# Performance work log

Measured on AMD Instinct MI355X. Metric: run time of the kernel, lower is better.

Reference implementation:

```python
import jax, jax.numpy as jnp
import numpy as np

DIM = 2048
N_HEADS = 32
N_KV_HEADS = 8
HEAD_DIM = DIM // N_HEADS
ROPE_BASE = 10000.0
BATCH = 2
SEQ = 2048


def _rope_cos_sin(seq_len, dtype=jnp.float32):
    inv_freq = 1.0 / (ROPE_BASE ** (jnp.arange(0, HEAD_DIM, 2, dtype=jnp.float32) / HEAD_DIM))
    pos = jnp.arange(seq_len, dtype=jnp.float32)
    freqs = pos[:, None] * inv_freq[None, :]  # (seq, head_dim/2)
    return jnp.cos(freqs).astype(dtype), jnp.sin(freqs).astype(dtype)


def _apply_rope(x, cos, sin):
    # x: (b, h, s, d); cos/sin: (s, d/2). Interleaved (even/odd) RoPE.
    cos = cos[None, None, :, :]
    sin = sin[None, None, :, :]
    x_even = x[..., ::2]
    x_odd = x[..., 1::2]
    rot_even = x_even * cos - x_odd * sin
    rot_odd = x_even * sin + x_odd * cos
    out = jnp.stack((rot_even, rot_odd), axis=-1)
    return out.reshape(x.shape)


def setup_inputs() -> dict:
    key = jax.random.key(0)
    ks = jax.random.split(key, 5)
    s = 0.02
    return {
        "x": jax.random.normal(ks[0], (BATCH, SEQ, DIM), dtype=jnp.float32),
        "wq": jax.random.normal(ks[1], (DIM, N_HEADS * HEAD_DIM), dtype=jnp.float32) * s,
        "wk": jax.random.normal(ks[2], (DIM, N_KV_HEADS * HEAD_DIM), dtype=jnp.float32) * s,
        "wv": jax.random.normal(ks[3], (DIM, N_KV_HEADS * HEAD_DIM), dtype=jnp.float32) * s,
        "wo": jax.random.normal(ks[4], (DIM, DIM), dtype=jnp.float32) * s,
    }


def reference(x, wq, wk, wv, wo):
    b, s, _ = x.shape
    q = (x @ wq).reshape(b, s, N_HEADS, HEAD_DIM).transpose(0, 2, 1, 3)
    k = (x @ wk).reshape(b, s, N_KV_HEADS, HEAD_DIM).transpose(0, 2, 1, 3)
    v = (x @ wv).reshape(b, s, N_KV_HEADS, HEAD_DIM).transpose(0, 2, 1, 3)
    cos, sin = _rope_cos_sin(s, x.dtype)
    q = _apply_rope(q, cos, sin)
    k = _apply_rope(k, cos, sin)
    rep = N_HEADS // N_KV_HEADS
    if rep > 1:
        k = jnp.repeat(k, rep, axis=1)
        v = jnp.repeat(v, rep, axis=1)
    scores = jnp.einsum("bhqd,bhkd->bhqk", q, k) / (HEAD_DIM ** 0.5)
    causal = jnp.tril(jnp.ones((s, s), dtype=bool))
    scores = jnp.where(causal[None, None], scores, -jnp.inf)
    probs = jax.nn.softmax(scores, axis=-1)
    out = jnp.einsum("bhqk,bhkd->bhqd", probs, v)
    out = out.transpose(0, 2, 1, 3).reshape(b, s, DIM)
    return out @ wo
```

## Files before the change

kernel.cpp:

```cpp
#include <hip/hip_runtime.h>
#include <stdint.h>

#define DIM   2048
#define NH    32
#define NKV   8
#define HD    64
#define BATCH 2
#define SEQ   2048

typedef __attribute__((ext_vector_type(8))) short  short8;
typedef __attribute__((ext_vector_type(4))) short  short4v;
typedef __attribute__((ext_vector_type(4))) float  f32x4;

#if __has_builtin(__builtin_amdgcn_exp2f)
#define EXP2(x) __builtin_amdgcn_exp2f(x)
#else
#define EXP2(x) exp2f(x)
#endif

static __device__ __forceinline__ short f2bf(float f) {
  union { float f; uint32_t u; } v; v.f = f;
  uint32_t r = v.u + 0x7FFFu + ((v.u >> 16) & 1u);
  return (short)(r >> 16);
}

static __device__ __forceinline__ uint32_t cvtpk_bf16(float lo, float hi) {
  uint32_t r;
  asm("v_cvt_pk_bf16_f32 %0, %1, %2" : "=v"(r) : "v"(lo), "v"(hi));
  return r;
}

#define GLD16(gp, lp) __builtin_amdgcn_global_load_lds(                      \
    (__attribute__((address_space(1))) void*)(void*)(gp),                    \
    (__attribute__((address_space(3))) void*)(lp), 16, 0, 0)

#define QSCALE 0.1803368801111244f


__global__ void cvt_x_kernel(const float* __restrict__ in, short* __restrict__ out, int n4) {
  int i = blockIdx.x * blockDim.x + threadIdx.x;
  if (i < n4) {
    f32x4 v = *reinterpret_cast<const f32x4*>(in + (size_t)i * 4);
    short4v o;
    o.x = f2bf(v.x); o.y = f2bf(v.y); o.z = f2bf(v.z); o.w = f2bf(v.w);
    *reinterpret_cast<short4v*>(out + (size_t)i * 4) = o;
  }
}

__global__ void transpose_bf_kernel(const float* __restrict__ in, short* __restrict__ out,
                                    int R, int C) {
  __shared__ float t[32][33];
  int c0 = blockIdx.x * 32, r0 = blockIdx.y * 32;
  int tx = threadIdx.x, ty = threadIdx.y;
#pragma unroll
  for (int j = 0; j < 32; j += 8)
    t[ty + j][tx] = in[(size_t)(r0 + ty + j) * C + c0 + tx];
  __syncthreads();
#pragma unroll
  for (int j = 0; j < 32; j += 8)
    out[(size_t)(c0 + ty + j) * R + r0 + tx] = f2bf(t[tx][ty + j]);
}

__global__ void rope_tab_kernel(float* __restrict__ ct, float* __restrict__ st) {
  int i = blockIdx.x * blockDim.x + threadIdx.x;
  if (i < SEQ * 32) {
    int pos = i >> 5, f = i & 31;
    float inv = powf(10000.0f, -(float)f / 32.0f);
    float th = (float)pos * inv;
    ct[i] = cosf(th);
    st[i] = sinf(th);
  }
}


__device__ __forceinline__ void mfma_tile(const short* __restrict__ as_,
                                          const short* __restrict__ bs_,
                                          int wr, int wc, int lg, int lr,
                                          f32x4 (&acc)[4][4]) {
  short8 af[4], bq[4];
#pragma unroll
  for (int mt = 0; mt < 4; ++mt) {
    int row = wr * 64 + mt * 16 + lr;
    af[mt] = *(const short8*)&as_[row * 32 + ((lg ^ ((row >> 1) & 3)) << 3)];
  }
#pragma unroll
  for (int nt = 0; nt < 4; ++nt) {
    int row = wc * 64 + nt * 16 + lr;
    bq[nt] = *(const short8*)&bs_[row * 32 + ((lg ^ ((row >> 1) & 3)) << 3)];
  }
  __builtin_amdgcn_s_setprio(1);
#pragma unroll
  for (int mt = 0; mt < 4; ++mt)
#pragma unroll
    for (int nt = 0; nt < 4; ++nt)
      acc[mt][nt] = __builtin_amdgcn_mfma_f32_16x16x32_bf16(af[mt], bq[nt], acc[mt][nt], 0, 0, 0);
  __builtin_amdgcn_s_setprio(0);
}

#define STAGE4(SA, SB) do {                                                  \
    GLD16(pA0, (SA) + w * 512);  GLD16(pA1, (SA) + 2048 + w * 512);          \
    GLD16(pB0, (SB) + w * 512);  GLD16(pB1, (SB) + 2048 + w * 512);          \
    pA0 += 32; pA1 += 32; pB0 += 32; pB1 += 32; } while (0)

#define TILE(CA, CB, SA, SB, DOSTAGE, VM) do {                               \
    asm volatile("s_waitcnt vmcnt(" VM ")" ::: "memory");                    \
    __builtin_amdgcn_s_barrier();                                            \
    __builtin_amdgcn_sched_barrier(0);                                       \
    if (DOSTAGE) { STAGE4(SA, SB); }                                         \
    mfma_tile(CA, CB, wr, wc, lg, lr, acc);                                  \
  } while (0)

__device__ __forceinline__ void gemm_mainloop(const short* __restrict__ A,
                                              const short* __restrict__ Bt,
                                              int m0, int n0,
                                              short* As, short* Bs,
                                              f32x4 (&acc)[4][4]) {
  const int tid = threadIdx.x;
  const int w = tid >> 6, l = tid & 63;
  const int lg = l >> 4, lr = l & 15;
  const int wr = w >> 1, wc = w & 1;
  const int c1 = tid + 256;
  const int r0 = tid >> 2, k0 = ((tid & 3) ^ ((r0 >> 1) & 3)) << 3;
  const int r1 = c1 >> 2,  k1 = ((c1 & 3) ^ ((r1 >> 1) & 3)) << 3;
  const short* pA0 = A + (size_t)(m0 + r0) * DIM + k0;
  const short* pA1 = A + (size_t)(m0 + r1) * DIM + k1;
  const short* pB0 = Bt + (size_t)(n0 + r0) * DIM + k0;
  const short* pB1 = Bt + (size_t)(n0 + r1) * DIM + k1;
  short* A0 = As;            short* B0 = Bs;
  short* A1 = As + 4096;     short* B1 = Bs + 4096;
  short* A2 = As + 8192;     short* B2 = Bs + 8192;

  STAGE4(A0, B0);
  STAGE4(A1, B1);

  for (int it = 0; it < 20; ++it) {
    TILE(A0, B0, A2, B2, true, "4");
    TILE(A1, B1, A0, B0, true, "4");
    TILE(A2, B2, A1, B1, true, "4");
  }
  TILE(A0, B0, A2, B2, true,  "4");
  TILE(A1, B1, A0, B0, true,  "4");
  TILE(A2, B2, A0, B0, false, "4");
  TILE(A0, B0, A1, B1, false, "0");
}

__device__ __forceinline__ int2 xcd_swizzle(int nwg) {
  int id = blockIdx.y * gridDim.x + blockIdx.x;
  int swz = (id & 7) * (nwg >> 3) + (id >> 3);
  return make_int2(swz % gridDim.x, swz / gridDim.x);
}

__global__ void __launch_bounds__(256, 3)
gemm_qkv_kernel(const short* __restrict__ A,
                const short* __restrict__ wqt, const short* __restrict__ wkt,
                const short* __restrict__ wvt,
                short* __restrict__ q_ws, short* __restrict__ k_ws, short* __restrict__ v_ws,
                const float* __restrict__ ct, const float* __restrict__ st) {
  __shared__ __align__(16) short As[12288];
  __shared__ __align__(16) short Bs[12288];
  int2 bxy = xcd_swizzle(24 * 32);
  const int n0g = bxy.x * 128;
  const int m0 = bxy.y * 128;
  int mode, n0;
  const short* Bt;
  short* outp;
  if (n0g < 2048)      { mode = 1; Bt = wqt; n0 = n0g;        outp = q_ws; }
  else if (n0g < 2560) { mode = 2; Bt = wkt; n0 = n0g - 2048; outp = k_ws; }
  else                 { mode = 3; Bt = wvt; n0 = n0g - 2560; outp = v_ws; }

  f32x4 acc[4][4] = {};
  gemm_mainloop(A, Bt, m0, n0, As, Bs, acc);

  const int tid = threadIdx.x;
  const int w = tid >> 6, l = tid & 63;
  const int lg = l >> 4, lr = l & 15;
  const int wr = w >> 1, wc = w & 1;
  const int mrow0 = m0 + wr * 64;
  const int ncol0 = n0 + wc * 64;
#pragma unroll
  for (int mt = 0; mt < 4; ++mt)
#pragma unroll
    for (int nt = 0; nt < 4; ++nt)
#pragma unroll
      for (int i = 0; i < 4; ++i) {
        int m = mrow0 + mt * 16 + lg * 4 + i;
        int n = ncol0 + nt * 16 + lr;
        float v = acc[mt][nt][i];
        int b = m >> 11, s = m & (SEQ - 1);
        int h = n >> 6, d = n & 63;
        if (mode == 3) {
          outp[((size_t)(b * NKV + h) * HD + d) * SEQ + s] = f2bf(v);
        } else {
          float p = __shfl_xor(v, 1);
          float cs = ct[(s << 5) + (d >> 1)];
          float sn = st[(s << 5) + (d >> 1)];
          float r = ((d & 1) == 0) ? (v * cs - p * sn) : (p * sn + v * cs);
          if (mode == 1) {
            r *= QSCALE;
            outp[((size_t)(b * NH + h) * SEQ + s) * HD + d] = f2bf(r);
          } else {
            outp[((size_t)(b * NKV + h) * SEQ + s) * HD + d] = f2bf(r);
          }
        }
      }
}

__global__ void __launch_bounds__(256, 3)
gemm_o_kernel(const short* __restrict__ A, const short* __restrict__ Bt,
              float* __restrict__ out) {
  __shared__ __align__(16) short As[12288];
  __shared__ __align__(16) short Bs[12288];
  int2 bxy = xcd_swizzle(16 * 32);
  const int m0 = bxy.y * 128, n0 = bxy.x * 128;
  f32x4 acc[4][4] = {};
  gemm_mainloop(A, Bt, m0, n0, As, Bs, acc);
  const int tid = threadIdx.x;
  const int w = tid >> 6, l = tid & 63;
  const int lg = l >> 4, lr = l & 15;
  const int wr = w >> 1, wc = w & 1;
#pragma unroll
  for (int mt = 0; mt < 4; ++mt)
#pragma unroll
    for (int nt = 0; nt < 4; ++nt)
#pragma unroll
      for (int i = 0; i < 4; ++i) {
        int m = m0 + wr * 64 + mt * 16 + lg * 4 + i;
        int n = n0 + wc * 64 + nt * 16 + lr;
        out[(size_t)m * DIM + n] = acc[mt][nt][i];
      }
}

__global__ void __launch_bounds__(256, 3)
attn_fwd_kernel(const short* __restrict__ Q, const short* __restrict__ K,
                const short* __restrict__ V, short* __restrict__ O) {
  __shared__ __align__(16) short Ks[3][4096];
  __shared__ __align__(16) short Vs[3][4096];
  const int tid = threadIdx.x;
  const int w = tid >> 6, l = tid & 63;
  const int lg = l >> 4, lr = l & 15;
  const int h = blockIdx.y;
  const int b = blockIdx.z;
  const int kvh = h >> 2;
  const int lh = lg >> 1, sub = (lg & 1) << 2;

  const short* kbase = K + (size_t)(b * NKV + kvh) * SEQ * HD;
  const short* vbase = V + (size_t)(b * NKV + kvh) * HD * SEQ;

  const int c1 = tid + 256;
  const int r0 = tid >> 3, e0 = ((tid & 7) ^ (r0 & 7)) << 3;
  const int r1 = c1 >> 3, e1 = ((c1 & 7) ^ (r1 & 7)) << 3;

  short8 ones;
#pragma unroll
  for (int i = 0; i < 8; ++i) ones[i] = (short)0x3F80;

#define ASTAGE(kvt, KB, VB) do { const int kv_ = (kvt) * 64;                  \
    GLD16(kbase + (size_t)(kv_ + r0) * HD + e0, (KB) + w * 512);              \
    GLD16(kbase + (size_t)(kv_ + r1) * HD + e1, (KB) + 2048 + w * 512);       \
    GLD16(vbase + (size_t)r0 * SEQ + kv_ + e0, (VB) + w * 512);               \
    GLD16(vbase + (size_t)r1 * SEQ + kv_ + e1, (VB) + 2048 + w * 512); } while (0)

  for (int qi = 0; qi < 2; ++qi) {
    const int qblk = (qi == 0) ? (int)blockIdx.x : (31 - (int)blockIdx.x);
    const int q0 = qblk * 64;
    const int qrow = q0 + w * 16 + lr;

    const short* qptr = Q + ((size_t)(b * NH + h) * SEQ + qrow) * HD;
    short8 qf0 = *(const short8*)(qptr + (lg << 3));
    short8 qf1 = *(const short8*)(qptr + 32 + (lg << 3));

    float m_run = 0.f;
    f32x4 oacc[4] = {};
    f32x4 lacc = {};

    short* kb0 = Ks[0]; short* kb1 = Ks[1]; short* kb2 = Ks[2];
    short* vb0 = Vs[0]; short* vb1 = Vs[1]; short* vb2 = Vs[2];

    ASTAGE(0, kb0, vb0);
    if (qblk >= 1) ASTAGE(1, kb1, vb1);

    for (int t = 0; t <= qblk; ++t) {
      if (t < qblk) asm volatile("s_waitcnt vmcnt(4)" ::: "memory");
      else          asm volatile("s_waitcnt vmcnt(0)" ::: "memory");
      __builtin_amdgcn_s_barrier();
      __builtin_amdgcn_sched_barrier(0);
      if (t + 2 <= qblk) ASTAGE(t + 2, kb2, vb2);

      const short* ks = kb0;
      const short* vs = vb0;
      const int kv0 = t * 64;

      short8 ka[4][2];
#pragma unroll
      for (int t4 = 0; t4 < 4; ++t4) {
        int row = t4 * 16 + lr, rx = row & 7;
        ka[t4][0] = *(const short8*)&ks[row * 64 + ((lg ^ rx) << 3)];
        ka[t4][1] = *(const short8*)&ks[row * 64 + (((4 + lg) ^ rx) << 3)];
      }
      short8 vbf[4][2];
#pragma unroll
      for (int nt = 0; nt < 4; ++nt) {
        int row = nt * 16 + lr, rx = row & 7;
#pragma unroll
        for (int ks_ = 0; ks_ < 2; ++ks_) {
          union { short8 s8; short4v hh[2]; } u;
          u.hh[0] = *(const short4v*)&vs[row * 64 + (((4 * ks_ + lh) ^ rx) << 3) + sub];
          u.hh[1] = *(const short4v*)&vs[row * 64 + (((4 * ks_ + 2 + lh) ^ rx) << 3) + sub];
          vbf[nt][ks_] = u.s8;
        }
      }

      f32x4 sacc[4];
      {
        f32x4 seed;
        seed[0] = -m_run; seed[1] = -m_run; seed[2] = -m_run; seed[3] = -m_run;
        __builtin_amdgcn_s_setprio(1);
#pragma unroll
        for (int t4 = 0; t4 < 4; ++t4) {
          f32x4 z = __builtin_amdgcn_mfma_f32_16x16x32_bf16(ka[t4][0], qf0, seed, 0, 0, 0);
          sacc[t4] = __builtin_amdgcn_mfma_f32_16x16x32_bf16(ka[t4][1], qf1, z, 0, 0, 0);
        }
        __builtin_amdgcn_s_setprio(0);
      }

      if (t == qblk) {
#pragma unroll
        for (int t4 = 0; t4 < 4; ++t4)
#pragma unroll
          for (int i = 0; i < 4; ++i)
            if (kv0 + t4 * 16 + lg * 4 + i > qrow) sacc[t4][i] = -__builtin_inff();
      }

      float a0 = fmaxf(fmaxf(sacc[0][0], sacc[0][1]), sacc[0][2]);
      float a1 = fmaxf(fmaxf(sacc[0][3], sacc[1][0]), sacc[1][1]);
      float a2 = fmaxf(fmaxf(sacc[1][2], sacc[1][3]), sacc[2][0]);
      float a3 = fmaxf(fmaxf(sacc[2][1], sacc[2][2]), sacc[2][3]);
      float a4 = fmaxf(fmaxf(sacc[3][0], sacc[3][1]), sacc[3][2]);
      float tm = fmaxf(fmaxf(fmaxf(a0, a1), a2), fmaxf(fmaxf(a3, a4), sacc[3][3]));
      tm = fmaxf(tm, __shfl_xor(tm, 16));
      tm = fmaxf(tm, __shfl_xor(tm, 32));

      if (!__all(tm <= 12.0f)) {
        float d = fmaxf(tm, 0.f);
        float alpha = EXP2(-d);
        float av0 = __shfl(alpha, (lg << 2));
        float av1 = __shfl(alpha, (lg << 2) | 1);
        float av2 = __shfl(alpha, (lg << 2) | 2);
        float av3 = __shfl(alpha, (lg << 2) | 3);
#pragma unroll
        for (int nt = 0; nt < 4; ++nt) {
          oacc[nt][0] *= av0; oacc[nt][1] *= av1;
          oacc[nt][2] *= av2; oacc[nt][3] *= av3;
        }
        lacc[0] *= av0; lacc[1] *= av1; lacc[2] *= av2; lacc[3] *= av3;
        m_run += d;
#pragma unroll
        for (int t4 = 0; t4 < 4; ++t4)
#pragma unroll
          for (int i = 0; i < 4; ++i) sacc[t4][i] -= d;
      }

      union { short8 s8; uint32_t u[4]; } pa0, pa1;
      pa0.u[0] = cvtpk_bf16(EXP2(sacc[0][0]), EXP2(sacc[0][1]));
      pa0.u[1] = cvtpk_bf16(EXP2(sacc[0][2]), EXP2(sacc[0][3]));
      pa0.u[2] = cvtpk_bf16(EXP2(sacc[1][0]), EXP2(sacc[1][1]));
      pa0.u[3] = cvtpk_bf16(EXP2(sacc[1][2]), EXP2(sacc[1][3]));
      pa1.u[0] = cvtpk_bf16(EXP2(sacc[2][0]), EXP2(sacc[2][1]));
      pa1.u[1] = cvtpk_bf16(EXP2(sacc[2][2]), EXP2(sacc[2][3]));
      pa1.u[2] = cvtpk_bf16(EXP2(sacc[3][0]), EXP2(sacc[3][1]));
      pa1.u[3] = cvtpk_bf16(EXP2(sacc[3][2]), EXP2(sacc[3][3]));

      __builtin_amdgcn_s_setprio(1);
#pragma unroll
      for (int nt = 0; nt < 4; ++nt) {
        oacc[nt] = __builtin_amdgcn_mfma_f32_16x16x32_bf16(pa0.s8, vbf[nt][0], oacc[nt], 0, 0, 0);
        oacc[nt] = __builtin_amdgcn_mfma_f32_16x16x32_bf16(pa1.s8, vbf[nt][1], oacc[nt], 0, 0, 0);
      }
      lacc = __builtin_amdgcn_mfma_f32_16x16x32_bf16(pa0.s8, ones, lacc, 0, 0, 0);
      lacc = __builtin_amdgcn_mfma_f32_16x16x32_bf16(pa1.s8, ones, lacc, 0, 0, 0);
      __builtin_amdgcn_s_setprio(0);

      short* tk = kb0; kb0 = kb1; kb1 = kb2; kb2 = tk;
      short* tv = vb0; vb0 = vb1; vb1 = vb2; vb2 = tv;
    }

    float linv0 = 1.f / lacc[0], linv1 = 1.f / lacc[1];
    float linv2 = 1.f / lacc[2], linv3 = 1.f / lacc[3];
#pragma unroll
    for (int nt = 0; nt < 4; ++nt) {
      int d = nt * 16 + lr;
      int qb = q0 + w * 16 + lg * 4;
      O[(size_t)(b * SEQ + qb + 0) * DIM + h * HD + d] = f2bf(oacc[nt][0] * linv0);
      O[(size_t)(b * SEQ + qb + 1) * DIM + h * HD + d] = f2bf(oacc[nt][1] * linv1);
      O[(size_t)(b * SEQ + qb + 2) * DIM + h * HD + d] = f2bf(oacc[nt][2] * linv2);
      O[(size_t)(b * SEQ + qb + 3) * DIM + h * HD + d] = f2bf(oacc[nt][3] * linv3);
    }
    __syncthreads();
  }
#undef ASTAGE
}


extern "C" void kernel_launch(void* const* d_in, const int* in_sizes, int n_in,
                              void* d_out, int out_size, void* d_ws, size_t ws_size,
                              hipStream_t stream) {
  const float* x  = (const float*)d_in[0];
  const float* wq = (const float*)d_in[1];
  const float* wk = (const float*)d_in[2];
  const float* wv = (const float*)d_in[3];
  const float* wo = (const float*)d_in[4];
  float* out = (float*)d_out;
  char* ws = (char*)d_ws;

  short* x_bf  = (short*)(ws + 0);
  short* attn  = (short*)(ws + 0);
  short* q_ws  = (short*)(ws + 16777216);
  short* k_ws  = (short*)(ws + 33554432);
  short* v_ws  = (short*)(ws + 37748736);
  short* wq_t  = (short*)(ws + 41943040);
  short* wo_t  = (short*)(ws + 41943040);
  short* wk_t  = (short*)(ws + 50331648);
  short* wv_t  = (short*)(ws + 52428800);
  float* ct    = (float*)(ws + 54525952);
  float* st    = (float*)(ws + 54788096);
  (void)ws_size; (void)in_sizes; (void)n_in; (void)out_size;

  dim3 tb(32, 8);
  cvt_x_kernel<<<8192, 256, 0, stream>>>(x, x_bf, 2097152);
  transpose_bf_kernel<<<dim3(64, 64), tb, 0, stream>>>(wq, wq_t, DIM, 2048);
  transpose_bf_kernel<<<dim3(16, 64), tb, 0, stream>>>(wk, wk_t, DIM, 512);
  transpose_bf_kernel<<<dim3(16, 64), tb, 0, stream>>>(wv, wv_t, DIM, 512);
  rope_tab_kernel<<<256, 256, 0, stream>>>(ct, st);

  gemm_qkv_kernel<<<dim3(24, 32), 256, 0, stream>>>(x_bf, wq_t, wk_t, wv_t,
                                                    q_ws, k_ws, v_ws, ct, st);

  attn_fwd_kernel<<<dim3(16, 32, 2), 256, 0, stream>>>(q_ws, k_ws, v_ws, attn);

  transpose_bf_kernel<<<dim3(64, 64), tb, 0, stream>>>(wo, wo_t, DIM, 2048);
  gemm_o_kernel<<<dim3(16, 32), 256, 0, stream>>>(attn, wo_t, out);
}
```

Before: 221.6 us.

## Replace GEMM mainloop with 8-wave 256-wide tiles and 4-phase double-buffered schedule

Both projection GEMMs switch from 128x128 tiles with 4 waves and a triple-buffered K=32 pipeline to larger tiles (256x256 for QKV, 128x256 for O) with 8 waves and K=64 double buffering. Each K step is split into four phases that interleave LDS fragment reads, global prefetch and MFMA quadrants under barriers. The larger tiles give more operand reuse per LDS load and fewer global reads. In exchange, LDS use and register pressure per block rise and the grids get smaller (192 and 256 blocks), which may underfill the 256 CUs and lower occupancy.

```diff
diff --git a/kernel.cpp b/kernel.cpp
--- a/kernel.cpp
+++ b/kernel.cpp
@@ -73,75 +73,109 @@
 }
 
 
-__device__ __forceinline__ void mfma_tile(const short* __restrict__ as_,
-                                          const short* __restrict__ bs_,
-                                          int wr, int wc, int lg, int lr,
-                                          f32x4 (&acc)[4][4]) {
-  short8 af[4], bq[4];
-#pragma unroll
-  for (int mt = 0; mt < 4; ++mt) {
-    int row = wr * 64 + mt * 16 + lr;
-    af[mt] = *(const short8*)&as_[row * 32 + ((lg ^ ((row >> 1) & 3)) << 3)];
-  }
-#pragma unroll
-  for (int nt = 0; nt < 4; ++nt) {
-    int row = wc * 64 + nt * 16 + lr;
-    bq[nt] = *(const short8*)&bs_[row * 32 + ((lg ^ ((row >> 1) & 3)) << 3)];
-  }
-  __builtin_amdgcn_s_setprio(1);
-#pragma unroll
-  for (int mt = 0; mt < 4; ++mt)
-#pragma unroll
-    for (int nt = 0; nt < 4; ++nt)
-      acc[mt][nt] = __builtin_amdgcn_mfma_f32_16x16x32_bf16(af[mt], bq[nt], acc[mt][nt], 0, 0, 0);
-  __builtin_amdgcn_s_setprio(0);
-}
-
-#define STAGE4(SA, SB) do {                                                  \
-    GLD16(pA0, (SA) + w * 512);  GLD16(pA1, (SA) + 2048 + w * 512);          \
-    GLD16(pB0, (SB) + w * 512);  GLD16(pB1, (SB) + 2048 + w * 512);          \
-    pA0 += 32; pA1 += 32; pB0 += 32; pB1 += 32; } while (0)
-
-#define TILE(CA, CB, SA, SB, DOSTAGE, VM) do {                               \
-    asm volatile("s_waitcnt vmcnt(" VM ")" ::: "memory");                    \
-    __builtin_amdgcn_s_barrier();                                            \
-    __builtin_amdgcn_sched_barrier(0);                                       \
-    if (DOSTAGE) { STAGE4(SA, SB); }                                         \
-    mfma_tile(CA, CB, wr, wc, lg, lr, acc);                                  \
-  } while (0)
-
-__device__ __forceinline__ void gemm_mainloop(const short* __restrict__ A,
-                                              const short* __restrict__ Bt,
-                                              int m0, int n0,
-                                              short* As, short* Bs,
-                                              f32x4 (&acc)[4][4]) {
+template <int BM, int BN, int WN>
+__device__ __forceinline__ void gemm_8ph(const short* __restrict__ A,
+                                         const short* __restrict__ Bt,
+                                         int m0, int n0,
+                                         short* __restrict__ As,
+                                         short* __restrict__ Bs,
+                                         f32x4 (&acc)[BM / ((8 / WN) * 16)][BN / (WN * 16)]) {
+  constexpr int WM = 8 / WN;
+  constexpr int MREP = BM / (WM * 16);
+  constexpr int NREP = BN / (WN * 16);
+  constexpr int MR2 = MREP / 2, NR2 = NREP / 2;
+  constexpr int APASS = BM / 64, BPASS = BN / 64;
+  constexpr int ABUF = BM * 64, BBUF = BN * 64;
+  constexpr int NT = DIM / 64;
+
   const int tid = threadIdx.x;
   const int w = tid >> 6, l = tid & 63;
   const int lg = l >> 4, lr = l & 15;
-  const int wr = w >> 1, wc = w & 1;
-  const int c1 = tid + 256;
-  const int r0 = tid >> 2, k0 = ((tid & 3) ^ ((r0 >> 1) & 3)) << 3;
-  const int r1 = c1 >> 2,  k1 = ((c1 & 3) ^ ((r1 >> 1) & 3)) << 3;
-  const short* pA0 = A + (size_t)(m0 + r0) * DIM + k0;
-  const short* pA1 = A + (size_t)(m0 + r1) * DIM + k1;
-  const short* pB0 = Bt + (size_t)(n0 + r0) * DIM + k0;
-  const short* pB1 = Bt + (size_t)(n0 + r1) * DIM + k1;
-  short* A0 = As;            short* B0 = Bs;
-  short* A1 = As + 4096;     short* B1 = Bs + 4096;
-  short* A2 = As + 8192;     short* B2 = Bs + 8192;
-
-  STAGE4(A0, B0);
-  STAGE4(A1, B1);
-
-  for (int it = 0; it < 20; ++it) {
-    TILE(A0, B0, A2, B2, true, "4");
-    TILE(A1, B1, A0, B0, true, "4");
-    TILE(A2, B2, A1, B1, true, "4");
+  const int wr = w / WN, wc = w % WN;
+  const int srow = tid >> 3;
+  const int su2 = (tid & 7) ^ (srow & 7);
+  const short* pA0 = A + (size_t)(m0 + srow) * DIM + su2 * 8;
+  const short* pB0 = Bt + (size_t)(n0 + srow) * DIM + su2 * 8;
+
+  auto stageA = [&](int t, int buf) {
+#pragma unroll
+    for (int p = 0; p < APASS; ++p)
+      GLD16(pA0 + (size_t)p * 64 * DIM + t * 64, As + buf * ABUF + p * 4096 + w * 512);
+  };
+  auto stageB = [&](int t, int buf) {
+#pragma unroll
+    for (int p = 0; p < BPASS; ++p)
+      GLD16(pB0 + (size_t)p * 64 * DIM + t * 64, Bs + buf * BBUF + p * 4096 + w * 512);
+  };
+
+  short8 af[MR2][2], bf0[NR2][2], bf1[NR2][2];
+
+  auto readA = [&](int mh, const short* base) {
+#pragma unroll
+    for (int i = 0; i < MR2; ++i) {
+      const int row = wr * (MREP * 16) + (mh * MR2 + i) * 16 + lr;
+#pragma unroll
+      for (int kk = 0; kk < 2; ++kk)
+        af[i][kk] = *(const short8*)&base[row * 64 + (((kk * 4 + lg) ^ (row & 7)) << 3)];
+    }
+  };
+  auto readB = [&](short8 (&bf)[NR2][2], int nh, const short* base) {
+#pragma unroll
+    for (int j = 0; j < NR2; ++j) {
+      const int row = wc * (NREP * 16) + (nh * NR2 + j) * 16 + lr;
+#pragma unroll
+      for (int kk = 0; kk < 2; ++kk)
+        bf[j][kk] = *(const short8*)&base[row * 64 + (((kk * 4 + lg) ^ (row & 7)) << 3)];
+    }
+  };
+  auto mmaQ = [&](short8 (&bf)[NR2][2], int mh, int nh) {
+    __builtin_amdgcn_s_setprio(1);
+#pragma unroll
+    for (int i = 0; i < MR2; ++i)
+#pragma unroll
+      for (int j = 0; j < NR2; ++j)
+#pragma unroll
+        for (int kk = 0; kk < 2; ++kk)
+          acc[mh * MR2 + i][nh * NR2 + j] = __builtin_amdgcn_mfma_f32_16x16x32_bf16(
+              af[i][kk], bf[j][kk], acc[mh * MR2 + i][nh * NR2 + j], 0, 0, 0);
+    __builtin_amdgcn_s_setprio(0);
+  };
+
+#define PH_SYNC do { __builtin_amdgcn_s_barrier();                           \
+    asm volatile("s_waitcnt lgkmcnt(0)" ::: "memory");                       \
+    __builtin_amdgcn_sched_barrier(0); } while (0)
+
+  stageA(0, 0);
+  stageB(0, 0);
+  asm volatile("s_waitcnt vmcnt(0)" ::: "memory");
+  __builtin_amdgcn_s_barrier();
+
+  for (int t = 0; t < NT; ++t) {
+    const int cur = t & 1;
+    const short* ab = As + cur * ABUF;
+    const short* bb = Bs + cur * BBUF;
+    const bool more = (t + 1 < NT);
+    readA(0, ab);
+    readB(bf0, 0, bb);
+    if (more) stageA(t + 1, cur ^ 1);
+    PH_SYNC;
+    mmaQ(bf0, 0, 0);
+    __builtin_amdgcn_s_barrier();
+    readB(bf1, 1, bb);
+    if (more) stageB(t + 1, cur ^ 1);
+    PH_SYNC;
+    mmaQ(bf1, 0, 1);
+    __builtin_amdgcn_s_barrier();
+    readA(1, ab);
+    PH_SYNC;
+    mmaQ(bf0, 1, 0);
+    __builtin_amdgcn_s_barrier();
+    PH_SYNC;
+    mmaQ(bf1, 1, 1);
+    asm volatile("s_waitcnt vmcnt(0)" ::: "memory");
+    __builtin_amdgcn_s_barrier();
   }
-  TILE(A0, B0, A2, B2, true,  "4");
-  TILE(A1, B1, A0, B0, true,  "4");
-  TILE(A2, B2, A0, B0, false, "4");
-  TILE(A0, B0, A1, B1, false, "0");
+#undef PH_SYNC
 }
 
 __device__ __forceinline__ int2 xcd_swizzle(int nwg) {
@@ -150,17 +184,17 @@
   return make_int2(swz % gridDim.x, swz / gridDim.x);
 }
 
-__global__ void __launch_bounds__(256, 3)
+__global__ void __launch_bounds__(512, 2)
 gemm_qkv_kernel(const short* __restrict__ A,
                 const short* __restrict__ wqt, const short* __restrict__ wkt,
                 const short* __restrict__ wvt,
                 short* __restrict__ q_ws, short* __restrict__ k_ws, short* __restrict__ v_ws,
                 const float* __restrict__ ct, const float* __restrict__ st) {
-  __shared__ __align__(16) short As[12288];
-  __shared__ __align__(16) short Bs[12288];
-  int2 bxy = xcd_swizzle(24 * 32);
-  const int n0g = bxy.x * 128;
-  const int m0 = bxy.y * 128;
+  __shared__ __align__(16) short As[2 * 256 * 64];
+  __shared__ __align__(16) short Bs[2 * 256 * 64];
+  int2 bxy = xcd_swizzle(12 * 16);
+  const int n0g = bxy.x * 256;
+  const int m0 = bxy.y * 256;
   int mode, n0;
   const short* Bt;
   short* outp;
@@ -168,17 +202,17 @@
   else if (n0g < 2560) { mode = 2; Bt = wkt; n0 = n0g - 2048; outp = k_ws; }
   else                 { mode = 3; Bt = wvt; n0 = n0g - 2560; outp = v_ws; }
 
-  f32x4 acc[4][4] = {};
-  gemm_mainloop(A, Bt, m0, n0, As, Bs, acc);
+  f32x4 acc[8][4] = {};
+  gemm_8ph<256, 256, 4>(A, Bt, m0, n0, As, Bs, acc);
 
   const int tid = threadIdx.x;
   const int w = tid >> 6, l = tid & 63;
   const int lg = l >> 4, lr = l & 15;
-  const int wr = w >> 1, wc = w & 1;
-  const int mrow0 = m0 + wr * 64;
+  const int wr = w >> 2, wc = w & 3;
+  const int mrow0 = m0 + wr * 128;
   const int ncol0 = n0 + wc * 64;
 #pragma unroll
-  for (int mt = 0; mt < 4; ++mt)
+  for (int mt = 0; mt < 8; ++mt)
 #pragma unroll
     for (int nt = 0; nt < 4; ++nt)
 #pragma unroll
@@ -205,19 +239,19 @@
       }
 }
 
-__global__ void __launch_bounds__(256, 3)
+__global__ void __launch_bounds__(512, 2)
 gemm_o_kernel(const short* __restrict__ A, const short* __restrict__ Bt,
               float* __restrict__ out) {
-  __shared__ __align__(16) short As[12288];
-  __shared__ __align__(16) short Bs[12288];
-  int2 bxy = xcd_swizzle(16 * 32);
-  const int m0 = bxy.y * 128, n0 = bxy.x * 128;
+  __shared__ __align__(16) short As[2 * 128 * 64];
+  __shared__ __align__(16) short Bs[2 * 256 * 64];
+  int2 bxy = xcd_swizzle(8 * 32);
+  const int m0 = bxy.y * 128, n0 = bxy.x * 256;
   f32x4 acc[4][4] = {};
-  gemm_mainloop(A, Bt, m0, n0, As, Bs, acc);
+  gemm_8ph<128, 256, 4>(A, Bt, m0, n0, As, Bs, acc);
   const int tid = threadIdx.x;
   const int w = tid >> 6, l = tid & 63;
   const int lg = l >> 4, lr = l & 15;
-  const int wr = w >> 1, wc = w & 1;
+  const int wr = w >> 2, wc = w & 3;
 #pragma unroll
   for (int mt = 0; mt < 4; ++mt)
 #pragma unroll
@@ -432,11 +466,11 @@
   transpose_bf_kernel<<<dim3(16, 64), tb, 0, stream>>>(wv, wv_t, DIM, 512);
   rope_tab_kernel<<<256, 256, 0, stream>>>(ct, st);
 
-  gemm_qkv_kernel<<<dim3(24, 32), 256, 0, stream>>>(x_bf, wq_t, wk_t, wv_t,
+  gemm_qkv_kernel<<<dim3(12, 16), 512, 0, stream>>>(x_bf, wq_t, wk_t, wv_t,
                                                     q_ws, k_ws, v_ws, ct, st);
 
   attn_fwd_kernel<<<dim3(16, 32, 2), 256, 0, stream>>>(q_ws, k_ws, v_ws, attn);
 
   transpose_bf_kernel<<<dim3(64, 64), tb, 0, stream>>>(wo, wo_t, DIM, 2048);
-  gemm_o_kernel<<<dim3(16, 32), 256, 0, stream>>>(attn, wo_t, out);
-}
+  gemm_o_kernel<<<dim3(8, 32), 512, 0, stream>>>(attn, wo_t, out);
+}
```

After: 230.5 us. +4.0%, slower.
